# Kernel optimization log

Measured on AMD Instinct MI355X. Metric: run time of the kernel, lower is better.

The kernel has to match this reference:

```python
import jax, jax.numpy as jnp
import numpy as np

B, S, D, H = 2, 512, 512, 8
HD = D // H  # 64


def setup_inputs() -> dict:
    key = jax.random.key(0)
    ks = jax.random.split(key, 14)
    sd = 1.0 / np.sqrt(D)
    sh = 1.0 / np.sqrt(HD)
    return {
        "query": jax.random.normal(ks[0], (B, S, D), jnp.float32),
        "key_": jax.random.normal(ks[1], (B, S, D), jnp.float32),
        "value": jax.random.normal(ks[2], (B, S, D), jnp.float32),
        "Wq": jax.random.uniform(ks[3], (D, D), jnp.float32, -sd, sd),
        "bq": jax.random.uniform(ks[4], (D,), jnp.float32, -sd, sd),
        "Wk": jax.random.uniform(ks[5], (D, D), jnp.float32, -sd, sd),
        "bk": jax.random.uniform(ks[6], (D,), jnp.float32, -sd, sd),
        "Wv": jax.random.uniform(ks[7], (D, D), jnp.float32, -sd, sd),
        "bv": jax.random.uniform(ks[8], (D,), jnp.float32, -sd, sd),
        "Wo": jax.random.uniform(ks[9], (D, D), jnp.float32, -sd, sd),
        "bo": jax.random.uniform(ks[10], (D,), jnp.float32, -sd, sd),
        "Aq": jax.random.uniform(ks[11], (HD, HD), jnp.float32, -sh, sh),
        "Ak": jax.random.uniform(ks[12], (HD, HD), jnp.float32, -sh, sh),
        "av": jax.random.normal(ks[13], (HD,), jnp.float32) * sh,
    }


def _heads(x):
    b, s, _ = x.shape
    return x.reshape(b, s, H, HD).transpose(0, 2, 1, 3)  # [b,h,s,hd]


def reference(query, key_, value, Wq, bq, Wk, bk, Wv, bv, Wo, bo, Aq, Ak, av):
    q = _heads(query @ Wq + bq)   # [b,h,q,hd]
    k = _heads(key_ @ Wk + bk)    # [b,h,k,hd]
    v = _heads(value @ Wv + bv)   # [b,h,k,hd]
    # additive (Bahdanau-style) scores: tanh(add_q(q)[:,:,:,None]+add_k(k)[:,:,None]) . av
    q_term = (q @ Aq)[:, :, :, None, :]   # [b,h,q,1,hd]
    k_term = (k @ Ak)[:, :, None, :, :]   # [b,h,1,k,hd]
    scores = jnp.einsum('bhqkd,d->bhqk', jnp.tanh(q_term + k_term), av)
    attn_weights = jax.nn.softmax(scores, axis=-1)  # dropout is identity at eval
    ctx = jnp.einsum('bhqk,bhkd->bhqd', attn_weights, v)
    b, _, s, _ = ctx.shape
    ctx = ctx.transpose(0, 2, 1, 3).reshape(b, s, D)
    out = ctx @ Wo + bo
    return out, attn_weights
```

## Files before the change

kernel.cpp:

```cpp
#include <hip/hip_runtime.h>
#include <math.h>

#define Bb 2
#define Ss 512
#define Dd 512
#define Hh 8
#define HDd 64
#define BS (Bb*Ss)

#if __has_builtin(__builtin_amdgcn_exp2f)
#define EXP2F(x) __builtin_amdgcn_exp2f(x)
#else
#define EXP2F(x) exp2f(x)
#endif
#if __has_builtin(__builtin_amdgcn_rcpf)
#define RCPF(x) __builtin_amdgcn_rcpf(x)
#else
#define RCPF(x) (1.0f/(x))
#endif

typedef float v4f __attribute__((ext_vector_type(4)));
typedef short v8s __attribute__((ext_vector_type(8)));

struct HL { short h, l; };

__device__ __forceinline__ HL split1(float x) {
  unsigned u = __builtin_bit_cast(unsigned, x);
  unsigned h = (u + 0x7fffu + ((u >> 16) & 1u)) >> 16;
  float hf = __builtin_bit_cast(float, h << 16);
  float lo = x - hf;
  unsigned ul = __builtin_bit_cast(unsigned, lo);
  unsigned l = (ul + 0x7fffu + ((ul >> 16) & 1u)) >> 16;
  HL r; r.h = (short)h; r.l = (short)l;
  return r;
}

__device__ __forceinline__ void split8p(const float* __restrict__ xp, v8s& ah, v8s& al) {
#pragma unroll
  for (int j = 0; j < 8; j++) {
    const HL r = split1(xp[j]);
    ah[j] = r.h; al[j] = r.l;
  }
}

__device__ __forceinline__ void split8v(float4 x0, float4 x1, v8s& ah, v8s& al) {
  HL r;
  r = split1(x0.x); ah[0] = r.h; al[0] = r.l;
  r = split1(x0.y); ah[1] = r.h; al[1] = r.l;
  r = split1(x0.z); ah[2] = r.h; al[2] = r.l;
  r = split1(x0.w); ah[3] = r.h; al[3] = r.l;
  r = split1(x1.x); ah[4] = r.h; al[4] = r.l;
  r = split1(x1.y); ah[5] = r.h; al[5] = r.l;
  r = split1(x1.z); ah[6] = r.h; al[6] = r.l;
  r = split1(x1.w); ah[7] = r.h; al[7] = r.l;
}

__global__ __launch_bounds__(256) void qkv_all(
    const float* __restrict__ Xq, const float* __restrict__ Xk, const float* __restrict__ Xv,
    const float* __restrict__ Wq, const float* __restrict__ Wk, const float* __restrict__ Wv,
    const float* __restrict__ Wo,
    const float* __restrict__ bq, const float* __restrict__ bk, const float* __restrict__ bv,
    const float* __restrict__ Aq, const float* __restrict__ Ak,
    float* __restrict__ EQ, float* __restrict__ EKt, float* __restrict__ Vw,
    short* __restrict__ WoPk)
{
  __shared__ __align__(16) short fragH[2][4][64][8];
  __shared__ __align__(16) short fragL[2][4][64][8];
  __shared__ float qs[64][68];
  __shared__ float qs2[16][260];

  const int z = blockIdx.z;
  const float* X    = (z == 0) ? Xq : (z == 1) ? Xk : Xv;
  const float* W    = (z == 0) ? Wq : (z == 1) ? Wk : Wv;
  const float* bias = (z == 0) ? bq : (z == 1) ? bk : bv;
  const int tid = threadIdx.x, l = tid & 63, w = tid >> 6;
  const int lm = l & 15, lq = l >> 4;
  const int h = blockIdx.x;
  const int r0 = blockIdx.y * 64;

  v4f acc[4] = {{0.f,0.f,0.f,0.f},{0.f,0.f,0.f,0.f},{0.f,0.f,0.f,0.f},{0.f,0.f,0.f,0.f}};
  const float* xrow = X + (size_t)(r0 + w * 16 + lm) * Dd + lq * 8;

  for (int kt = 0; kt < 16; ++kt) {
    const int buf = kt & 1;
    const float4 xa0 = *(const float4*)&xrow[kt * 32];
    const float4 xa1 = *(const float4*)&xrow[kt * 32 + 4];
    {
      v8s hh, ll;
#pragma unroll
      for (int j = 0; j < 8; j++) {
        const float x = W[(size_t)(kt * 32 + lq * 8 + j) * Dd + h * 64 + w * 16 + lm];
        const HL r = split1(x);
        hh[j] = r.h; ll[j] = r.l;
      }
      *(v8s*)&fragH[buf][w][l][0] = hh;
      *(v8s*)&fragL[buf][w][l][0] = ll;
    }
    __syncthreads();
    v8s ah, al;
    split8v(xa0, xa1, ah, al);
#pragma unroll
    for (int t = 0; t < 4; t++) {
      const v8s bh = *(const v8s*)&fragH[buf][t][l][0];
      const v8s bl = *(const v8s*)&fragL[buf][t][l][0];
      acc[t] = __builtin_amdgcn_mfma_f32_16x16x32_bf16(ah, bh, acc[t], 0, 0, 0);
      acc[t] = __builtin_amdgcn_mfma_f32_16x16x32_bf16(ah, bl, acc[t], 0, 0, 0);
      acc[t] = __builtin_amdgcn_mfma_f32_16x16x32_bf16(al, bh, acc[t], 0, 0, 0);
    }
  }

  if (z == 2) {
#pragma unroll
    for (int t = 0; t < 4; t++) {
      const int n = h * 64 + t * 16 + lm;
      const float bvv = bias[n];
#pragma unroll
      for (int r = 0; r < 4; r++)
        Vw[(size_t)(r0 + w * 16 + lq * 4 + r) * Dd + n] = acc[t][r] + bvv;
    }
    {
      const int tau = (blockIdx.y * 8 + h) * 4 + w;
      const int nt = tau >> 4, kt = tau & 15;
      v8s hh, ll;
#pragma unroll
      for (int j = 0; j < 8; j++) {
        const float x = Wo[(size_t)(kt * 32 + lq * 8 + j) * Dd + nt * 16 + lm];
        const HL r = split1(x);
        hh[j] = r.h; ll[j] = r.l;
      }
      *(v8s*)&WoPk[((size_t)tau * 64 + l) * 16 + 0] = hh;
      *(v8s*)&WoPk[((size_t)tau * 64 + l) * 16 + 8] = ll;
    }
    return;
  }

#pragma unroll
  for (int t = 0; t < 4; t++) {
    const int n = h * 64 + t * 16 + lm;
    const float bvv = bias[n];
#pragma unroll
    for (int r = 0; r < 4; r++)
      qs[w * 16 + lq * 4 + r][t * 16 + lm] = acc[t][r] + bvv;
  }
  __syncthreads();

  const float* Am = (z == 0) ? Aq : Ak;
  v4f a2[4] = {{0.f,0.f,0.f,0.f},{0.f,0.f,0.f,0.f},{0.f,0.f,0.f,0.f},{0.f,0.f,0.f,0.f}};
#pragma unroll
  for (int kt2 = 0; kt2 < 2; ++kt2) {
    v8s ah, al;
    split8p(&qs[w * 16 + lm][kt2 * 32 + lq * 8], ah, al);
#pragma unroll
    for (int t2 = 0; t2 < 4; t2++) {
      v8s bh, bl;
#pragma unroll
      for (int j = 0; j < 8; j++) {
        const float x = Am[(kt2 * 32 + lq * 8 + j) * HDd + t2 * 16 + lm]
                        * 2.885390081777927f;
        const HL r = split1(x);
        bh[j] = r.h; bl[j] = r.l;
      }
      a2[t2] = __builtin_amdgcn_mfma_f32_16x16x32_bf16(ah, bh, a2[t2], 0, 0, 0);
      a2[t2] = __builtin_amdgcn_mfma_f32_16x16x32_bf16(ah, bl, a2[t2], 0, 0, 0);
      a2[t2] = __builtin_amdgcn_mfma_f32_16x16x32_bf16(al, bh, a2[t2], 0, 0, 0);
    }
  }

  if (z == 0) {
#pragma unroll
    for (int t2 = 0; t2 < 4; t2++)
#pragma unroll
      for (int rr = 0; rr < 4; rr++)
        EQ[(size_t)(r0 + w * 16 + lq * 4 + rr) * Dd + h * 64 + t2 * 16 + lm] = EXP2F(a2[t2][rr]);
  } else {
#pragma unroll
    for (int t2 = 0; t2 < 4; t2++)
#pragma unroll
      for (int rr = 0; rr < 4; rr++)
        qs2[4 * t2 + (lm >> 2)][(w * 16 + lq * 4 + rr) * 4 + (lm & 3)] = EXP2F(a2[t2][rr]);
    __syncthreads();
    const int b = r0 >> 9;
    const size_t base = (size_t)(b * 8 + h) * 16 * 2048 + (size_t)(r0 & 511) * 4;
#pragma unroll
    for (int i = 0; i < 4; i++) {
      const int f = i * 1024 + tid * 4;
      const int dt = f >> 8, c = f & 255;
      *(float4*)&EKt[base + (size_t)dt * 2048 + c] = *(const float4*)&qs2[dt][c];
    }
  }
}

__device__ __forceinline__ float grp4(v4f e, v4f ek, v4f av4) {
  const float A = __builtin_fmaf(e.x, ek.x, 1.f);
  const float B = __builtin_fmaf(e.y, ek.y, 1.f);
  const float C = __builtin_fmaf(e.z, ek.z, 1.f);
  const float D = __builtin_fmaf(e.w, ek.w, 1.f);
  const float AB = A * B;
  const float CD = C * D;
  const float n1 = __builtin_fmaf(av4.y, A, av4.x * B);
  const float n2 = __builtin_fmaf(av4.w, C, av4.z * D);
  const float N = __builtin_fmaf(n2, AB, n1 * CD);
  return N * RCPF(AB * CD);
}

__global__ __launch_bounds__(256) void attn_kernel(
    const float* __restrict__ EQ, const float* __restrict__ EKt,
    const float* __restrict__ V, const float* __restrict__ av,
    float* __restrict__ attnW, float* __restrict__ CTX)
{
  __shared__ float uni[16384];
  __shared__ float eq_s[16][64];
  __shared__ float avn[64];

  const int tid = threadIdx.x, l = tid & 63, w = tid >> 6;
  const int q0 = blockIdx.x * 16;
  const int bh = blockIdx.y;
  const int b = bh >> 3, h = bh & 7;

  {
    const int f = tid * 4, r = f >> 6, d = f & 63;
    *(float4*)&eq_s[r][d] =
        *(const float4*)&EQ[(size_t)(b * Ss + q0 + r) * Dd + h * HDd + d];
    if (tid < 64) avn[tid] = -2.f * av[tid];
  }

  const float* ekbase = EKt + (size_t)bh * 16 * 2048;
  {
    float4 pre[8];
#pragma unroll
    for (int j = 0; j < 8; j++)
      pre[j] = *(const float4*)&ekbase[j * 1024 + tid * 4];
#pragma unroll
    for (int j = 0; j < 8; j++)
      *(float4*)&uni[j * 1024 + tid * 4] = pre[j];
  }
  __syncthreads();

  const int qg = w * 4;
  float a[4][8];
#pragma unroll
  for (int j = 0; j < 4; j++)
#pragma unroll
    for (int kg = 0; kg < 8; kg++) a[j][kg] = 0.f;

#pragma unroll 1
  for (int ch = 0; ch < 4; ++ch) {
    const int cb = (ch & 1) * 8192;
    const int nb = ((ch + 1) & 1) * 8192;
    const int chn = (ch < 3) ? ch + 1 : 3;
    float4 pre[8];
#pragma unroll
    for (int j = 0; j < 8; j++)
      pre[j] = *(const float4*)&ekbase[(size_t)chn * 8192 + j * 1024 + tid * 4];

#pragma unroll
    for (int s = 0; s < 4; ++s) {
      const int dt = ch * 4 + s;
      const v4f av4 = *(const v4f*)&avn[dt * 4];
      const v4f e0 = *(const v4f*)&eq_s[qg + 0][dt * 4];
      const v4f e1 = *(const v4f*)&eq_s[qg + 1][dt * 4];
      const v4f e2 = *(const v4f*)&eq_s[qg + 2][dt * 4];
      const v4f e3 = *(const v4f*)&eq_s[qg + 3][dt * 4];
#pragma unroll
      for (int kg = 0; kg < 8; kg++) {
        const v4f ek = *(const v4f*)&uni[cb + s * 2048 + kg * 256 + l * 4];
        a[0][kg] += grp4(e0, ek, av4);
        a[1][kg] += grp4(e1, ek, av4);
        a[2][kg] += grp4(e2, ek, av4);
        a[3][kg] += grp4(e3, ek, av4);
      }
    }
#pragma unroll
    for (int j = 0; j < 8; j++)
      *(float4*)&uni[nb + j * 1024 + tid * 4] = pre[j];
    __syncthreads();
  }

#pragma unroll
  for (int j = 0; j < 4; j++) {
    float m = -1e30f;
#pragma unroll
    for (int kg = 0; kg < 8; kg++) m = fmaxf(m, a[j][kg]);
#pragma unroll
    for (int off = 32; off >= 1; off >>= 1) m = fmaxf(m, __shfl_xor(m, off, 64));
    float s = 0.f;
#pragma unroll
    for (int kg = 0; kg < 8; kg++) {
      a[j][kg] = EXP2F((a[j][kg] - m) * 1.4426950408889634f);
      s += a[j][kg];
    }
#pragma unroll
    for (int off = 32; off >= 1; off >>= 1) s += __shfl_xor(s, off, 64);
    const float inv = RCPF(s);
    float* arow = attnW + ((size_t)bh * Ss + q0 + qg + j) * Ss;
#pragma unroll
    for (int kg = 0; kg < 8; kg++) {
      const float wv = a[j][kg] * inv;
      uni[(qg + j) * 516 + kg * 64 + l] = wv;
      arow[kg * 64 + l] = wv;
    }
  }
  __syncthreads();

  {
    const int cq = tid >> 4;
    const int dq = (tid & 15) * 4;
    const float* vb = V + (size_t)b * Ss * Dd + h * HDd + dq;
    const float* scr = &uni[cq * 516];
    v4f o = {0.f, 0.f, 0.f, 0.f};
    for (int kk = 0; kk < Ss; kk += 2) {
      const float2 wv = *(const float2*)&scr[kk];
      const v4f v0 = *(const v4f*)&vb[(size_t)kk * Dd];
      const v4f v1 = *(const v4f*)&vb[(size_t)(kk + 1) * Dd];
      o += wv.x * v0 + wv.y * v1;
    }
    *(v4f*)&CTX[(size_t)(b * Ss + q0 + cq) * Dd + h * HDd + dq] = o;
  }
}

__global__ __launch_bounds__(256) void out_pk(
    const float* __restrict__ CTX, const short* __restrict__ WoPk,
    const float* __restrict__ bo, float* __restrict__ out)
{
  const int tid = threadIdx.x;
  const int l = tid & 63, w = tid >> 6;
  const int lm = l & 15, lq = l >> 4;
  const int m0 = blockIdx.y * 64 + w * 16;
  const int nt0 = blockIdx.x * 4;

  v4f acc[4] = {{0.f,0.f,0.f,0.f},{0.f,0.f,0.f,0.f},{0.f,0.f,0.f,0.f},{0.f,0.f,0.f,0.f}};
  const float* xrow = CTX + (size_t)(m0 + lm) * Dd + lq * 8;

#pragma unroll 2
  for (int kt = 0; kt < 16; ++kt) {
    v8s ah, al;
    split8p(xrow + kt * 32, ah, al);
#pragma unroll
    for (int t = 0; t < 4; t++) {
      const int tau = (nt0 + t) * 16 + kt;
      const size_t bi = ((size_t)tau * 64 + l) * 16;
      const v8s bh = *(const v8s*)&WoPk[bi + 0];
      const v8s bl = *(const v8s*)&WoPk[bi + 8];
      acc[t] = __builtin_amdgcn_mfma_f32_16x16x32_bf16(ah, bh, acc[t], 0, 0, 0);
      acc[t] = __builtin_amdgcn_mfma_f32_16x16x32_bf16(ah, bl, acc[t], 0, 0, 0);
      acc[t] = __builtin_amdgcn_mfma_f32_16x16x32_bf16(al, bh, acc[t], 0, 0, 0);
    }
  }
#pragma unroll
  for (int t = 0; t < 4; t++) {
    const int n = (nt0 + t) * 16 + lm;
    const float bv = bo[n];
#pragma unroll
    for (int r = 0; r < 4; r++)
      out[(size_t)(m0 + lq * 4 + r) * Dd + n] = acc[t][r] + bv;
  }
}

extern "C" void kernel_launch(void* const* d_in, const int* in_sizes, int n_in,
                              void* d_out, int out_size, void* d_ws, size_t ws_size,
                              hipStream_t stream) {
  (void)in_sizes; (void)n_in; (void)out_size; (void)ws_size;
  const float* query = (const float*)d_in[0];
  const float* key_  = (const float*)d_in[1];
  const float* value = (const float*)d_in[2];
  const float* Wq    = (const float*)d_in[3];
  const float* bq    = (const float*)d_in[4];
  const float* Wk    = (const float*)d_in[5];
  const float* bk    = (const float*)d_in[6];
  const float* Wv    = (const float*)d_in[7];
  const float* bv    = (const float*)d_in[8];
  const float* Wo    = (const float*)d_in[9];
  const float* bo    = (const float*)d_in[10];
  const float* Aq    = (const float*)d_in[11];
  const float* Ak    = (const float*)d_in[12];
  const float* av    = (const float*)d_in[13];

  float* outp = (float*)d_out;
  float* attn = outp + (size_t)BS * Dd;

  float* ws  = (float*)d_ws;
  float* EQ  = ws;
  float* EKt = ws + (size_t)BS * Dd;
  float* Vw  = ws + 2 * (size_t)BS * Dd;
  float* CTX = ws + 3 * (size_t)BS * Dd;
  short* WoPk = (short*)(ws + 4 * (size_t)BS * Dd);

  qkv_all<<<dim3(8, 16, 3), 256, 0, stream>>>(query, key_, value,
      Wq, Wk, Wv, Wo, bq, bk, bv, Aq, Ak, EQ, EKt, Vw, WoPk);
  attn_kernel<<<dim3(32, 16), 256, 0, stream>>>(EQ, EKt, Vw, av, attn, CTX);
  out_pk<<<dim3(8, 16), 256, 0, stream>>>(CTX, WoPk, bo, outp);
}
```

Measured before the change: 191.3 us.

## Stream EK tiles via direct global-to-LDS loads with smaller double buffer

Replaces the register-staged 4-chunk prefetch of the EK tensor in the attention kernel with per-d-tile direct global-to-LDS loads (global_load_lds builtin), using a 2x2048-float double buffer. This shrinks LDS from 64KB to about 33KB, which may raise occupancy, and frees the 32 prefetch registers. It also loads the EQ tile by the same direct path and rewrites grp4 to use a vector FMA for the denominators. The trade-off is 16 barriers instead of 4, and no explicit wait on the asynchronous LDS writes before the barrier, so the path relies on compiler-inserted vmcnt waits.

```diff
diff --git a/kernel.cpp b/kernel.cpp
--- a/kernel.cpp
+++ b/kernel.cpp
@@ -54,6 +54,19 @@
   r = split1(x1.z); ah[6] = r.h; al[6] = r.l;
   r = split1(x1.w); ah[7] = r.h; al[7] = r.l;
 }
+
+#if __has_builtin(__builtin_amdgcn_global_load_lds)
+__device__ __forceinline__ void gl2lds16(const float* g, float* l) {
+  __builtin_amdgcn_global_load_lds(
+      (const __attribute__((address_space(1))) void*)g,
+      (__attribute__((address_space(3))) void*)l, 16, 0, 0);
+}
+#else
+__device__ __forceinline__ void gl2lds16(const float* g, float* l) {
+  const int lane = threadIdx.x & 63;
+  *(float4*)((char*)l + lane * 16) = *(const float4*)g;
+}
+#endif
 
 __global__ __launch_bounds__(256) void qkv_all(
     const float* __restrict__ Xq, const float* __restrict__ Xk, const float* __restrict__ Xv,
@@ -191,14 +204,12 @@
 }
 
 __device__ __forceinline__ float grp4(v4f e, v4f ek, v4f av4) {
-  const float A = __builtin_fmaf(e.x, ek.x, 1.f);
-  const float B = __builtin_fmaf(e.y, ek.y, 1.f);
-  const float C = __builtin_fmaf(e.z, ek.z, 1.f);
-  const float D = __builtin_fmaf(e.w, ek.w, 1.f);
-  const float AB = A * B;
-  const float CD = C * D;
-  const float n1 = __builtin_fmaf(av4.y, A, av4.x * B);
-  const float n2 = __builtin_fmaf(av4.w, C, av4.z * D);
+  const v4f one = {1.f, 1.f, 1.f, 1.f};
+  const v4f den = e * ek + one;
+  const float AB = den.x * den.y;
+  const float CD = den.z * den.w;
+  const float n1 = __builtin_fmaf(av4.y, den.x, av4.x * den.y);
+  const float n2 = __builtin_fmaf(av4.w, den.z, av4.z * den.w);
   const float N = __builtin_fmaf(n2, AB, n1 * CD);
   return N * RCPF(AB * CD);
 }
@@ -208,8 +219,8 @@
     const float* __restrict__ V, const float* __restrict__ av,
     float* __restrict__ attnW, float* __restrict__ CTX)
 {
-  __shared__ float uni[16384];
-  __shared__ float eq_s[16][64];
+  __shared__ __align__(16) float uni[8256];
+  __shared__ __align__(16) float eq_s[16][64];
   __shared__ float avn[64];
 
   const int tid = threadIdx.x, l = tid & 63, w = tid >> 6;
@@ -218,22 +229,15 @@
   const int b = bh >> 3, h = bh & 7;
 
   {
-    const int f = tid * 4, r = f >> 6, d = f & 63;
-    *(float4*)&eq_s[r][d] =
-        *(const float4*)&EQ[(size_t)(b * Ss + q0 + r) * Dd + h * HDd + d];
-    if (tid < 64) avn[tid] = -2.f * av[tid];
-  }
+    const float* eqg = EQ + (size_t)(b * Ss + q0 + w * 4 + (l >> 4)) * Dd
+                       + h * HDd + (l & 15) * 4;
+    gl2lds16(eqg, &eq_s[w * 4][0]);
+  }
+  if (tid < 64) avn[tid] = -2.f * av[tid];
 
   const float* ekbase = EKt + (size_t)bh * 16 * 2048;
-  {
-    float4 pre[8];
-#pragma unroll
-    for (int j = 0; j < 8; j++)
-      pre[j] = *(const float4*)&ekbase[j * 1024 + tid * 4];
-#pragma unroll
-    for (int j = 0; j < 8; j++)
-      *(float4*)&uni[j * 1024 + tid * 4] = pre[j];
-  }
+  gl2lds16(ekbase + w * 512 + l * 4, &uni[w * 512]);
+  gl2lds16(ekbase + w * 512 + 256 + l * 4, &uni[w * 512 + 256]);
   __syncthreads();
 
   const int qg = w * 4;
@@ -244,35 +248,26 @@
     for (int kg = 0; kg < 8; kg++) a[j][kg] = 0.f;
 
 #pragma unroll 1
-  for (int ch = 0; ch < 4; ++ch) {
-    const int cb = (ch & 1) * 8192;
-    const int nb = ((ch + 1) & 1) * 8192;
-    const int chn = (ch < 3) ? ch + 1 : 3;
-    float4 pre[8];
-#pragma unroll
-    for (int j = 0; j < 8; j++)
-      pre[j] = *(const float4*)&ekbase[(size_t)chn * 8192 + j * 1024 + tid * 4];
-
-#pragma unroll
-    for (int s = 0; s < 4; ++s) {
-      const int dt = ch * 4 + s;
-      const v4f av4 = *(const v4f*)&avn[dt * 4];
-      const v4f e0 = *(const v4f*)&eq_s[qg + 0][dt * 4];
-      const v4f e1 = *(const v4f*)&eq_s[qg + 1][dt * 4];
-      const v4f e2 = *(const v4f*)&eq_s[qg + 2][dt * 4];
-      const v4f e3 = *(const v4f*)&eq_s[qg + 3][dt * 4];
-#pragma unroll
-      for (int kg = 0; kg < 8; kg++) {
-        const v4f ek = *(const v4f*)&uni[cb + s * 2048 + kg * 256 + l * 4];
-        a[0][kg] += grp4(e0, ek, av4);
-        a[1][kg] += grp4(e1, ek, av4);
-        a[2][kg] += grp4(e2, ek, av4);
-        a[3][kg] += grp4(e3, ek, av4);
-      }
-    }
-#pragma unroll
-    for (int j = 0; j < 8; j++)
-      *(float4*)&uni[nb + j * 1024 + tid * 4] = pre[j];
+  for (int dt = 0; dt < 16; ++dt) {
+    const int cb = (dt & 1) * 2048;
+    const int nb = 2048 - cb;
+    const int dtn = (dt < 15) ? dt + 1 : 15;
+    gl2lds16(ekbase + (size_t)dtn * 2048 + w * 512 + l * 4, &uni[nb + w * 512]);
+    gl2lds16(ekbase + (size_t)dtn * 2048 + w * 512 + 256 + l * 4, &uni[nb + w * 512 + 256]);
+
+    const v4f av4 = *(const v4f*)&avn[dt * 4];
+    const v4f e0 = *(const v4f*)&eq_s[qg + 0][dt * 4];
+    const v4f e1 = *(const v4f*)&eq_s[qg + 1][dt * 4];
+    const v4f e2 = *(const v4f*)&eq_s[qg + 2][dt * 4];
+    const v4f e3 = *(const v4f*)&eq_s[qg + 3][dt * 4];
+#pragma unroll
+    for (int kg = 0; kg < 8; kg++) {
+      const v4f ek = *(const v4f*)&uni[cb + kg * 256 + l * 4];
+      a[0][kg] += grp4(e0, ek, av4);
+      a[1][kg] += grp4(e1, ek, av4);
+      a[2][kg] += grp4(e2, ek, av4);
+      a[3][kg] += grp4(e3, ek, av4);
+    }
     __syncthreads();
   }
 
```

Measured after the change: 173.4 us. 9.4% less time.
